# Optimization experiments

Hardware: AMD Instinct MI355X
Metric: run time of the kernel (lower is better)

## Reference

```python
import jax, jax.numpy as jnp
import numpy as np

B, T_HIST, T_OUT, T_FC = 4096, 168, 48, 49
N_LABELS, F_CTL, F_FC, HID = 64, 16, 8, 32
EPS = 1e-7


def setup_inputs() -> dict:
    key = jax.random.key(0)
    ks = jax.random.split(key, 18)
    rn = lambda k, s, sc=1.0: jax.random.normal(k, s, jnp.float32) * sc
    return {
        "history": rn(ks[0], (B, T_HIST, N_LABELS)),
        "control": rn(ks[1], (B, T_OUT, F_CTL)),
        "forecasts": rn(ks[2], (B, T_FC, F_FC)),
        "h_mean": rn(ks[3], (N_LABELS,), 0.1),
        "h_var": jax.random.uniform(ks[4], (N_LABELS,), jnp.float32, 0.5, 1.5),
        "c_mean": rn(ks[5], (F_CTL,), 0.1),
        "c_var": jax.random.uniform(ks[6], (F_CTL,), jnp.float32, 0.5, 1.5),
        "f_mean": rn(ks[7], (), 0.1),
        "f_var": jax.random.uniform(ks[8], (), jnp.float32, 0.5, 1.5),
        "conv_w": rn(ks[9], (2, F_FC, 4), 0.2),   # kernel_size=2, Conv1D(4)
        "conv_b": rn(ks[10], (4,), 0.01),
        "lstm_k": rn(ks[11], (N_LABELS, 4 * HID), 0.1),
        "lstm_rk": rn(ks[12], (HID, 4 * HID), 0.1),
        "lstm_b": rn(ks[13], (4 * HID,), 0.01),
        "w1": rn(ks[14], (HID + F_CTL + 4, 64), 0.1),
        "b1": rn(ks[15], (64,), 0.01),
        "w2": rn(ks[16], (64, N_LABELS), 0.05),
        "b2": rn(ks[17], (N_LABELS,), 0.01),
    }


def _norm(x, m, v):
    # keras Normalization: (x - mean) / max(sqrt(var), eps)
    return (x - m) / jnp.maximum(jnp.sqrt(v), EPS)


def _lstm(x, h, c, k, rk, b):
    z = x @ k + h @ rk + b                      # [B, 4*HID], gate order i,f,g,o
    i, f, g, o = jnp.split(z, 4, axis=-1)
    c2 = jax.nn.sigmoid(f) * c + jax.nn.sigmoid(i) * jnp.tanh(g)
    h2 = jax.nn.sigmoid(o) * jnp.tanh(c2)
    return h2, c2


def _mlp(x1, x2, x3, w1, b1, w2, b2):
    x = jnp.concatenate([x1, x2, x3], axis=-1)  # [B, 52]
    return jax.nn.relu(x @ w1 + b1) @ w2 + b2


def reference(history, control, forecasts, h_mean, h_var, c_mean, c_var,
              f_mean, f_var, conv_w, conv_b, lstm_k, lstm_rk, lstm_b,
              w1, b1, w2, b2):
    latest = history[:, -1, :]                               # [B, N_LABELS]
    cn = _norm(control, c_mean, c_var)                       # [B, T_OUT, F_CTL]
    fn = _norm(forecasts, f_mean, f_var)                     # scalar norm
    # Conv1D(filters=4, kernel_size=2), valid padding -> [B, T_FC-1, 4]
    fc = fn[:, :-1] @ conv_w[0] + fn[:, 1:] @ conv_w[1] + conv_b

    # encoder LSTM over normalized history
    hn = _norm(history, h_mean, h_var)
    bsz = history.shape[0]
    init = (jnp.zeros((bsz, HID), hn.dtype), jnp.zeros((bsz, HID), hn.dtype))

    def enc_step(carry, x):
        h, c = carry
        return _lstm(x, h, c, lstm_k, lstm_rk, lstm_b), None

    (h, c), _ = jax.lax.scan(enc_step, init, jnp.swapaxes(hn, 0, 1))

    # pre-loop step (its prediction write is overwritten by loop i=0, but it
    # updates `latest` which feeds the loop)
    latest = latest + _mlp(h, cn[:, 0], fc[:, 0], w1, b1, w2, b2)

    t_out = control.shape[1]

    def dec_step(carry, inp):
        latest, h, c = carry
        ctl, fci = inp
        xn = _norm(latest, h_mean, h_var)
        h2, c2 = _lstm(xn, h, c, lstm_k, lstm_rk, lstm_b)
        latest2 = latest + _mlp(h2, ctl, fci, w1, b1, w2, b2)
        return (latest2, h2, c2), latest2

    xs = (jnp.swapaxes(cn, 0, 1), jnp.swapaxes(fc[:, :t_out], 0, 1))
    _, preds = jax.lax.scan(dec_step, (latest, h, c), xs)   # [T_OUT, B, N]
    return jnp.swapaxes(preds, 0, 1)                        # [B, T_OUT, N]
```

## Files before the change

kernel.cpp:

```cpp
#include <hip/hip_runtime.h>

#define EPSV 1e-7f

typedef __bf16 bf16x8 __attribute__((ext_vector_type(8)));
typedef float  f32x4  __attribute__((ext_vector_type(4)));
typedef unsigned int   u32x4 __attribute__((ext_vector_type(4)));
typedef unsigned short u16x8 __attribute__((ext_vector_type(8)));
typedef unsigned short u16x4 __attribute__((ext_vector_type(4)));

__device__ __forceinline__ unsigned short f2bf(float f) {
    unsigned int u = __float_as_uint(f);
    return (unsigned short)((u + 0x7FFFu + ((u >> 16) & 1u)) >> 16);
}
__device__ __forceinline__ float bf2f(unsigned short u) {
    return __uint_as_float(((unsigned int)u) << 16);
}
__device__ __forceinline__ void split2(float f, unsigned short& hi, unsigned short& lo) {
    hi = f2bf(f);
    lo = f2bf(f - bf2f(hi));
}
__device__ __forceinline__ void splitT(float f, unsigned short& hi, unsigned short& lo) {
    unsigned int u  = __float_as_uint(f);
    unsigned int hb = u & 0xFFFF0000u;
    float l = f - __uint_as_float(hb);
    hi = (unsigned short)(u >> 16);
    lo = (unsigned short)(__float_as_uint(l) >> 16);
}
__device__ __forceinline__ float sigf(float x) {
    return __builtin_amdgcn_rcpf(1.0f + __expf(-x));
}
__device__ __forceinline__ float tanhfast(float x) {
    float cx = fminf(fmaxf(x, -15.0f), 15.0f);
    float e = __expf(2.0f * cx);
    return (e - 1.0f) * __builtin_amdgcn_rcpf(e + 1.0f);
}
__device__ __forceinline__ float xor8(float v) {
    return __builtin_bit_cast(float, __builtin_amdgcn_update_dpp(
        0, __builtin_bit_cast(int, v), 0x128, 0xF, 0xF, true));
}

#define MFMA16(A, B, C) __builtin_amdgcn_mfma_f32_16x16x32_bf16(A, B, C, 0, 0, 0)
#define BC8(x) __builtin_bit_cast(bf16x8, x)

#define BARRIER() do {                                        \
    asm volatile("s_waitcnt lgkmcnt(0)" ::: "memory");        \
    __builtin_amdgcn_s_barrier();                             \
    __builtin_amdgcn_sched_barrier(0);                        \
} while (0)

#define HS2 72
#define MS  136
#define XS2 136
#define ZS3 20

__global__ __launch_bounds__(512, 1) void tutina_kernel(
    const float* __restrict__ history, const float* __restrict__ control,
    const float* __restrict__ forecasts,
    const float* __restrict__ h_mean, const float* __restrict__ h_var,
    const float* __restrict__ c_mean, const float* __restrict__ c_var,
    const float* __restrict__ f_mean, const float* __restrict__ f_var,
    const float* __restrict__ conv_w, const float* __restrict__ conv_b,
    const float* __restrict__ lstm_k, const float* __restrict__ lstm_rk,
    const float* __restrict__ lstm_b,
    const float* __restrict__ w1, const float* __restrict__ b1,
    const float* __restrict__ w2, const float* __restrict__ b2,
    float* __restrict__ out)
{
    __shared__ unsigned short hbuf[2][16 * HS2];
    __shared__ float zxb[2][4][2][16 * ZS3];
    __shared__ unsigned short xbuf[16 * XS2];
    __shared__ unsigned short mlps[16 * MS];
    __shared__ unsigned short hids[16 * MS];
    __shared__ unsigned int   fcs[48 * 64];

    const int tid  = threadIdx.x;
    const int lane = tid & 63;
    const int wid  = tid >> 6;
    const int wa   = wid & 3;
    const bool gA  = (wid < 4);
    const int lt   = tid & 255;
    const int l15  = lane & 15;
    const int l4   = lane >> 4;
    const int b0   = blockIdx.x * 16;

    for (int i = tid; i < 16 * HS2; i += 512) hbuf[0][i] = 0;
    for (int i = tid; i < 16 * MS;  i += 512) mlps[i] = 0;

    const int  uu     = l15 & 7;
    const bool lohalf = (l15 < 8);
    const int  u      = wa * 8 + uu;
    const int  jz0    = lohalf ? u      : 32 + u;
    const int  jz1    = lohalf ? 64 + u : 96 + u;
    const int  j1     = wa * 16 + l15;

    auto bfragK = [&](int kbase, int j, float& dacc, bf16x8& H, bf16x8& L) {
        u16x8 h, l;
#pragma unroll
        for (int i = 0; i < 8; i++) {
            int k = kbase + l4 * 8 + i;
            float sv = 1.0f / fmaxf(sqrtf(h_var[k]), EPSV);
            float w  = lstm_k[k * 128 + j] * sv;
            dacc += h_mean[k] * w;
            unsigned short hh, ll; split2(w, hh, ll);
            h[i] = hh; l[i] = ll;
        }
        H = BC8(h); L = BC8(l);
    };
    auto bfragP = [&](const float* W, int ldw, int kbase, int j, bf16x8& H, bf16x8& L) {
        u16x8 h, l;
#pragma unroll
        for (int i = 0; i < 8; i++) {
            int k = kbase + l4 * 8 + i;
            float w = W[k * ldw + j];
            unsigned short hh, ll; split2(w, hh, ll);
            h[i] = hh; l[i] = ll;
        }
        H = BC8(h); L = BC8(l);
    };
    auto bfragW11 = [&](int j, float& dacc, bf16x8& H, bf16x8& L) {
        u16x8 h, l;
#pragma unroll
        for (int i = 0; i < 8; i++) {
            int k = 32 + l4 * 8 + i;
            float w = 0.0f;
            if (k < 52) {
                w = w1[k * 64 + j];
                if (k < 48) {
                    float sv = 1.0f / fmaxf(sqrtf(c_var[k - 32]), EPSV);
                    w *= sv;
                    dacc += c_mean[k - 32] * w;
                }
            }
            unsigned short hh, ll; split2(w, hh, ll);
            h[i] = hh; l[i] = ll;
        }
        H = BC8(h); L = BC8(l);
    };

    bf16x8 fA0h, fA0l, fA1h, fA1l, fB0h, fB0l, fB1h, fB1l;
    float dz0 = 0.f, dz1 = 0.f;
    bfragK(0,  jz0, dz0, fA0h, fA0l);
    bfragK(32, jz0, dz0, fA1h, fA1l);
    bfragK(0,  jz1, dz1, fB0h, fB0l);
    bfragK(32, jz1, dz1, fB1h, fB1l);

    bf16x8 fA2h, fA2l, fB2h, fB2l;
    float bi_ = 0.f, bf_ = 0.f, bg_ = 0.f, bo_ = 0.f;
    if (gA) {
        bfragP(lstm_rk, 128, 0, jz0, fA2h, fA2l);
        bfragP(lstm_rk, 128, 0, jz1, fB2h, fB2l);
        float z0s = dz0, z1s = dz1;
        z0s += __shfl_xor(z0s, 16, 64); z0s += __shfl_xor(z0s, 32, 64);
        z1s += __shfl_xor(z1s, 16, 64); z1s += __shfl_xor(z1s, 32, 64);
        float pd0 = xor8(z0s), pd1 = xor8(z1s);
        bi_ = lstm_b[u]      - (lohalf ? z0s : pd0);
        bf_ = lstm_b[32 + u] - (lohalf ? pd0 : z0s);
        bg_ = lstm_b[64 + u] - (lohalf ? z1s : pd1);
        bo_ = lstm_b[96 + u] - (lohalf ? pd1 : z1s);
    }

    bf16x8 fW10h, fW10l, fW11h, fW11l, fW20h, fW20l, fW21h, fW21l;
    float b1j = 0.f, b2j = 0.f;
    float lat0 = 0.f, lat1 = 0.f, lat2 = 0.f, lat3 = 0.f;
    f32x4 creg = {0.f, 0.f, 0.f, 0.f};
    const int rc = lt >> 2, cc = (lt & 3) * 4;
    if (!gA) {
        bfragP(w1, 64, 0, j1, fW10h, fW10l);
        float d1 = 0.f;
        bfragW11(j1, d1, fW11h, fW11l);
        bfragP(w2, 64, 0,  j1, fW20h, fW20l);
        bfragP(w2, 64, 32, j1, fW21h, fW21l);
        d1 += __shfl_xor(d1, 16, 64); d1 += __shfl_xor(d1, 32, 64);
        b1j = b1[j1] - d1;
        b2j = b2[j1];
        lat0 = history[((size_t)(b0 + l4 * 4 + 0) * 168 + 167) * 64 + j1];
        lat1 = history[((size_t)(b0 + l4 * 4 + 1) * 168 + 167) * 64 + j1];
        lat2 = history[((size_t)(b0 + l4 * 4 + 2) * 168 + 167) * 64 + j1];
        lat3 = history[((size_t)(b0 + l4 * 4 + 3) * 168 + 167) * 64 + j1];
        if (lt < 64)
            creg = *(const f32x4*)(control + ((size_t)(b0 + rc) * 48 + 0) * 16 + cc);
        float fm  = f_mean[0];
        float fsc = 1.0f / fmaxf(sqrtf(f_var[0]), EPSV);
        for (int cell = lt; cell < 48 * 64; cell += 256) {
            int t  = cell >> 6;
            int b  = (cell >> 2) & 15;
            int uc = cell & 3;
            const float* fp = forecasts + ((size_t)(b0 + b) * 49 + t) * 8;
            float acc = conv_b[uc];
#pragma unroll
            for (int k = 0; k < 8; k++) {
                acc += (fp[k]     - fm) * fsc * conv_w[k * 4 + uc];
                acc += (fp[8 + k] - fm) * fsc * conv_w[32 + k * 4 + uc];
            }
            unsigned short hh, ll; split2(acc, hh, ll);
            fcs[cell] = ((unsigned int)hh << 16) | ll;
        }
    }

    const int r0 = l4 * 4 + (lohalf ? 0 : 2);
    const int r1 = r0 + 1;
    float c0 = 0.0f, c1 = 0.0f;

    auto lstm_gates = [&](const f32x4& a, const f32x4& b,
                          unsigned short* hw, bool write_mlp) {
        float sa0 = lohalf ? a[2] : a[0];
        float sa1 = lohalf ? a[3] : a[1];
        float sb0 = lohalf ? b[2] : b[0];
        float sb1 = lohalf ? b[3] : b[1];
        float ra0 = xor8(sa0);
        float ra1 = xor8(sa1);
        float rb0 = xor8(sb0);
        float rb1 = xor8(sb1);
        float zi0 = (lohalf ? a[0] : ra0) + bi_;
        float zi1 = (lohalf ? a[1] : ra1) + bi_;
        float zf0 = (lohalf ? ra0 : a[2]) + bf_;
        float zf1 = (lohalf ? ra1 : a[3]) + bf_;
        float zg0 = (lohalf ? b[0] : rb0) + bg_;
        float zg1 = (lohalf ? b[1] : rb1) + bg_;
        float zo0 = (lohalf ? rb0 : b[2]) + bo_;
        float zo1 = (lohalf ? rb1 : b[3]) + bo_;
        c0 = sigf(zf0) * c0 + sigf(zi0) * tanhfast(zg0);
        c1 = sigf(zf1) * c1 + sigf(zi1) * tanhfast(zg1);
        float h20 = sigf(zo0) * tanhfast(c0);
        float h21 = sigf(zo1) * tanhfast(c1);
        unsigned short bh, bl;
        splitT(h20, bh, bl);
        hw[r0 * HS2 + u]      = bh;
        hw[r0 * HS2 + 32 + u] = bl;
        if (write_mlp) { mlps[r0 * MS + u] = bh; mlps[r0 * MS + 64 + u] = bl; }
        splitT(h21, bh, bl);
        hw[r1 * HS2 + u]      = bh;
        hw[r1 * HS2 + 32 + u] = bl;
        if (write_mlp) { mlps[r1 * MS + u] = bh; mlps[r1 * MS + 64 + u] = bl; }
    };

    auto mk_frags = [&](const f32x4& p0, const f32x4& p1, const f32x4& p2,
                        const f32x4& p3, bf16x8& A0h, bf16x8& A0l,
                        bf16x8& A1h, bf16x8& A1l) {
        u16x8 xh_, xl_;
        unsigned short hh, ll;
#pragma unroll
        for (int i = 0; i < 4; i++) { splitT(p0[i], hh, ll); xh_[i] = hh; xl_[i] = ll; }
#pragma unroll
        for (int i = 0; i < 4; i++) { splitT(p1[i], hh, ll); xh_[4+i] = hh; xl_[4+i] = ll; }
        A0h = BC8(xh_); A0l = BC8(xl_);
#pragma unroll
        for (int i = 0; i < 4; i++) { splitT(p2[i], hh, ll); xh_[i] = hh; xl_[i] = ll; }
#pragma unroll
        for (int i = 0; i < 4; i++) { splitT(p3[i], hh, ll); xh_[4+i] = hh; xl_[4+i] = ll; }
        A1h = BC8(xh_); A1l = BC8(xl_);
    };
    auto zx12 = [&](bf16x8 A0h, bf16x8 A0l, bf16x8 A1h, bf16x8 A1l,
                    f32x4& zn0, f32x4& zn1) {
        f32x4 s0 = {0.f,0.f,0.f,0.f}, s1 = {0.f,0.f,0.f,0.f};
        s0 = MFMA16(A0h, fA0h, s0);  s1 = MFMA16(A0h, fB0h, s1);
        s0 = MFMA16(A1h, fA1h, s0);  s1 = MFMA16(A1h, fB1h, s1);
        s0 = MFMA16(A0l, fA0h, s0);  s1 = MFMA16(A0l, fB0h, s1);
        s0 = MFMA16(A1l, fA1h, s0);  s1 = MFMA16(A1l, fB1h, s1);
        s0 = MFMA16(A0h, fA0l, s0);  s1 = MFMA16(A0h, fB0l, s1);
        s0 = MFMA16(A1h, fA1l, s0);  s1 = MFMA16(A1h, fB1l, s1);
        zn0 = s0; zn1 = s1;
    };

    const float* hp = history + (size_t)(b0 + l15) * (168 * 64);
    const int o1 = l4 * 8, o2 = 32 + l4 * 8;
    const int zoff = l15 * ZS3 + l4 * 4;
    f32x4 vb0, vb1, vb2, vb3;
    if (!gA) {
        f32x4 p0 = *(const f32x4*)(hp + o1), p1 = *(const f32x4*)(hp + o1 + 4);
        f32x4 p2 = *(const f32x4*)(hp + o2), p3 = *(const f32x4*)(hp + o2 + 4);
        bf16x8 A0h, A0l, A1h, A1l;
        mk_frags(p0, p1, p2, p3, A0h, A0l, A1h, A1l);
        f32x4 zn0, zn1;
        zx12(A0h, A0l, A1h, A1l, zn0, zn1);
        *(f32x4*)&zxb[0][wa][0][zoff] = zn0;
        *(f32x4*)&zxb[0][wa][1][zoff] = zn1;
        vb0 = *(const f32x4*)(hp + 64 + o1); vb1 = *(const f32x4*)(hp + 64 + o1 + 4);
        vb2 = *(const f32x4*)(hp + 64 + o2); vb3 = *(const f32x4*)(hp + 64 + o2 + 4);
    }
    if (gA) __builtin_amdgcn_s_setprio(1);
    BARRIER();

    for (int t = 0; t < 168; ++t) {
        const int p = t & 1;
        if (gA) {
            const unsigned short* hr = hbuf[p];
            bf16x8 a2h = BC8(*(const u32x4*)&hr[l15 * HS2 + l4 * 8]);
            bf16x8 a2l = BC8(*(const u32x4*)&hr[l15 * HS2 + 32 + l4 * 8]);
            f32x4 z0 = *(const f32x4*)&zxb[p][wa][0][zoff];
            f32x4 z1 = *(const f32x4*)&zxb[p][wa][1][zoff];
            z0 = MFMA16(a2h, fA2h, z0);  z1 = MFMA16(a2h, fB2h, z1);
            z0 = MFMA16(a2l, fA2h, z0);  z1 = MFMA16(a2l, fB2h, z1);
            z0 = MFMA16(a2h, fA2l, z0);  z1 = MFMA16(a2h, fB2l, z1);
            lstm_gates(z0, z1, hbuf[p ^ 1], t == 167);
        } else {
            bf16x8 A0h, A0l, A1h, A1l;
            mk_frags(vb0, vb1, vb2, vb3, A0h, A0l, A1h, A1l);
            const float* np = hp + (size_t)((t < 166) ? t + 2 : 167) * 64;
            vb0 = *(const f32x4*)(np + o1); vb1 = *(const f32x4*)(np + o1 + 4);
            vb2 = *(const f32x4*)(np + o2); vb3 = *(const f32x4*)(np + o2 + 4);
            f32x4 zn0, zn1;
            zx12(A0h, A0l, A1h, A1l, zn0, zn1);
            *(f32x4*)&zxb[p ^ 1][wa][0][zoff] = zn0;
            *(f32x4*)&zxb[p ^ 1][wa][1][zoff] = zn1;
        }
        BARRIER();
    }

    auto stage_cn = [&](const f32x4& v) {
        if (lt < 64) {
            u16x4 oh, ol;
#pragma unroll
            for (int q = 0; q < 4; q++) {
                unsigned short hh, ll;
                splitT(v[q], hh, ll);
                oh[q] = hh; ol[q] = ll;
            }
            *(u16x4*)&mlps[rc * MS + 32 + cc]      = oh;
            *(u16x4*)&mlps[rc * MS + 64 + 32 + cc] = ol;
        }
    };
    auto stage_fc = [&](int t) {
        if (lt >= 64 && lt < 128) {
            int q = lt - 64;
            unsigned int v = fcs[t * 64 + q];
            mlps[(q >> 2) * MS + 48 + (q & 3)]      = (unsigned short)(v >> 16);
            mlps[(q >> 2) * MS + 64 + 48 + (q & 3)] = (unsigned short)(v & 0xFFFFu);
        }
    };
    auto mlp1 = [&]() {
        const int mbase = l15 * MS + l4 * 8;
        bf16x8 m0  = BC8(*(const u32x4*)&mlps[mbase]);
        bf16x8 m1  = BC8(*(const u32x4*)&mlps[mbase + 32]);
        bf16x8 m0l = BC8(*(const u32x4*)&mlps[mbase + 64]);
        bf16x8 m1l = BC8(*(const u32x4*)&mlps[mbase + 96]);
        f32x4 ha = {0.f,0.f,0.f,0.f}, hb = {0.f,0.f,0.f,0.f};
        ha = MFMA16(m0,  fW10h, ha);   hb = MFMA16(m1,  fW11h, hb);
        ha = MFMA16(m0l, fW10h, ha);   hb = MFMA16(m1l, fW11h, hb);
        ha = MFMA16(m0,  fW10l, ha);   hb = MFMA16(m1,  fW11l, hb);
        f32x4 hacc = ha + hb;
#pragma unroll
        for (int q = 0; q < 4; q++) {
            float hv = fmaxf(hacc[q] + b1j, 0.0f);
            unsigned short hh, ll;
            splitT(hv, hh, ll);
            hids[(l4 * 4 + q) * MS + j1]      = hh;
            hids[(l4 * 4 + q) * MS + 64 + j1] = ll;
        }
    };
    auto mlp2 = [&]() {
        const int mbase = l15 * MS + l4 * 8;
        bf16x8 h0  = BC8(*(const u32x4*)&hids[mbase]);
        bf16x8 h1  = BC8(*(const u32x4*)&hids[mbase + 32]);
        bf16x8 h0l = BC8(*(const u32x4*)&hids[mbase + 64]);
        bf16x8 h1l = BC8(*(const u32x4*)&hids[mbase + 96]);
        f32x4 oa = {0.f,0.f,0.f,0.f}, ob = {0.f,0.f,0.f,0.f};
        oa = MFMA16(h0,  fW20h, oa);   ob = MFMA16(h1,  fW21h, ob);
        oa = MFMA16(h0l, fW20h, oa);   ob = MFMA16(h1l, fW21h, ob);
        oa = MFMA16(h0,  fW20l, oa);   ob = MFMA16(h1,  fW21l, ob);
        f32x4 oacc = oa + ob;
        lat0 += oacc[0] + b2j;
        lat1 += oacc[1] + b2j;
        lat2 += oacc[2] + b2j;
        lat3 += oacc[3] + b2j;
    };

    if (!gA) { stage_cn(creg); stage_fc(0); }
    BARRIER();
    if (!gA) mlp1();
    BARRIER();
    if (!gA) mlp2();

    for (int t = 0; t < 48; ++t) {
        const int p = t & 1;
        if (!gA) {
            unsigned short bh, bl;
            splitT(lat0, bh, bl);
            xbuf[(l4 * 4 + 0) * XS2 + j1] = bh; xbuf[(l4 * 4 + 0) * XS2 + 64 + j1] = bl;
            splitT(lat1, bh, bl);
            xbuf[(l4 * 4 + 1) * XS2 + j1] = bh; xbuf[(l4 * 4 + 1) * XS2 + 64 + j1] = bl;
            splitT(lat2, bh, bl);
            xbuf[(l4 * 4 + 2) * XS2 + j1] = bh; xbuf[(l4 * 4 + 2) * XS2 + 64 + j1] = bl;
            splitT(lat3, bh, bl);
            xbuf[(l4 * 4 + 3) * XS2 + j1] = bh; xbuf[(l4 * 4 + 3) * XS2 + 64 + j1] = bl;
            stage_cn(creg);
            stage_fc(t);
            int tn = (t < 47) ? t + 1 : 47;
            if (lt < 64)
                creg = *(const f32x4*)(control + ((size_t)(b0 + rc) * 48 + tn) * 16 + cc);
        }
        BARRIER();

        if (gA) {
            const unsigned short* hr = hbuf[p];
            const int xb = l15 * XS2 + l4 * 8;
            bf16x8 a0h = BC8(*(const u32x4*)&xbuf[xb]);
            bf16x8 a1h = BC8(*(const u32x4*)&xbuf[xb + 32]);
            bf16x8 a0l = BC8(*(const u32x4*)&xbuf[xb + 64]);
            bf16x8 a1l = BC8(*(const u32x4*)&xbuf[xb + 96]);
            bf16x8 a2h = BC8(*(const u32x4*)&hr[l15 * HS2 + l4 * 8]);
            bf16x8 a2l = BC8(*(const u32x4*)&hr[l15 * HS2 + 32 + l4 * 8]);
            f32x4 z0a = {0.f,0.f,0.f,0.f}, z0b = {0.f,0.f,0.f,0.f};
            f32x4 z1a = {0.f,0.f,0.f,0.f}, z1b = {0.f,0.f,0.f,0.f};
            z0a = MFMA16(a0h, fA0h, z0a);  z1a = MFMA16(a0h, fB0h, z1a);
            z0b = MFMA16(a1h, fA1h, z0b);  z1b = MFMA16(a1h, fB1h, z1b);
            z0a = MFMA16(a2h, fA2h, z0a);  z1a = MFMA16(a2h, fB2h, z1a);
            z0b = MFMA16(a0l, fA0h, z0b);  z1b = MFMA16(a0l, fB0h, z1b);
            z0a = MFMA16(a1l, fA1h, z0a);  z1a = MFMA16(a1l, fB1h, z1a);
            z0b = MFMA16(a2l, fA2h, z0b);  z1b = MFMA16(a2l, fB2h, z1b);
            z0a = MFMA16(a0h, fA0l, z0a);  z1a = MFMA16(a0h, fB0l, z1a);
            z0b = MFMA16(a1h, fA1l, z0b);  z1b = MFMA16(a1h, fB1l, z1b);
            z0a = MFMA16(a2h, fA2l, z0a);  z1a = MFMA16(a2h, fB2l, z1a);
            f32x4 z0 = z0a + z0b, z1 = z1a + z1b;
            lstm_gates(z0, z1, hbuf[p ^ 1], true);
        }
        BARRIER();

        if (!gA) mlp1();
        BARRIER();

        if (!gA) {
            mlp2();
            out[((size_t)(b0 + l4 * 4 + 0) * 48 + t) * 64 + j1] = lat0;
            out[((size_t)(b0 + l4 * 4 + 1) * 48 + t) * 64 + j1] = lat1;
            out[((size_t)(b0 + l4 * 4 + 2) * 48 + t) * 64 + j1] = lat2;
            out[((size_t)(b0 + l4 * 4 + 3) * 48 + t) * 64 + j1] = lat3;
        }
    }
}

extern "C" void kernel_launch(void* const* d_in, const int* in_sizes, int n_in,
                              void* d_out, int out_size, void* d_ws, size_t ws_size,
                              hipStream_t stream) {
    tutina_kernel<<<dim3(256), dim3(512), 0, stream>>>(
        (const float*)d_in[0],  (const float*)d_in[1],  (const float*)d_in[2],
        (const float*)d_in[3],  (const float*)d_in[4],  (const float*)d_in[5],
        (const float*)d_in[6],  (const float*)d_in[7],  (const float*)d_in[8],
        (const float*)d_in[9],  (const float*)d_in[10], (const float*)d_in[11],
        (const float*)d_in[12], (const float*)d_in[13], (const float*)d_in[14],
        (const float*)d_in[15], (const float*)d_in[16], (const float*)d_in[17],
        (float*)d_out);
}
```

Baseline: 170.0 us.

## Move decoder MLP2 to LSTM warps, drop one per-step barrier, trim encoder h-lo MFMAs

Moves the second MLP layer and the running 'latest' state from the MLP warp group into the LSTM warps, with each LSTM warp holding w2 fragments for all 64 outputs. The x-staging now happens inside the LSTM phase behind a local LDS wait, which removes one block barrier per decoder step. The encoder recurrence drops the low-half bf16 correction term of h (fewer MFMAs and LDS writes), which lowers precision. The launch-bounds occupancy hint is raised to 2 blocks, which changes register-allocation pressure. The LSTM warps now repeat the MLP2 work redundantly, which adds register use.

```diff
diff --git a/kernel.cpp b/kernel.cpp
--- a/kernel.cpp
+++ b/kernel.cpp
@@ -47,13 +47,17 @@
     __builtin_amdgcn_s_barrier();                             \
     __builtin_amdgcn_sched_barrier(0);                        \
 } while (0)
+#define LGKM0() do {                                          \
+    asm volatile("s_waitcnt lgkmcnt(0)" ::: "memory");        \
+    __builtin_amdgcn_sched_barrier(0);                        \
+} while (0)
 
 #define HS2 72
 #define MS  136
 #define XS2 136
 #define ZS3 20
 
-__global__ __launch_bounds__(512, 1) void tutina_kernel(
+__global__ __launch_bounds__(512, 2) void tutina_kernel(
     const float* __restrict__ history, const float* __restrict__ control,
     const float* __restrict__ forecasts,
     const float* __restrict__ h_mean, const float* __restrict__ h_var,
@@ -145,6 +149,9 @@
     bfragK(32, jz1, dz1, fB1h, fB1l);
 
     bf16x8 fA2h, fA2l, fB2h, fB2l;
+    bf16x8 w2h0[4], w2l0[4], w2h1[4], w2l1[4];
+    float b2jm[4];
+    float lat[4][4];
     float bi_ = 0.f, bf_ = 0.f, bg_ = 0.f, bo_ = 0.f;
     if (gA) {
         bfragP(lstm_rk, 128, 0, jz0, fA2h, fA2l);
@@ -157,26 +164,24 @@
         bf_ = lstm_b[32 + u] - (lohalf ? pd0 : z0s);
         bg_ = lstm_b[64 + u] - (lohalf ? z1s : pd1);
         bo_ = lstm_b[96 + u] - (lohalf ? pd1 : z1s);
-    }
-
-    bf16x8 fW10h, fW10l, fW11h, fW11l, fW20h, fW20l, fW21h, fW21l;
-    float b1j = 0.f, b2j = 0.f;
-    float lat0 = 0.f, lat1 = 0.f, lat2 = 0.f, lat3 = 0.f;
+#pragma unroll
+        for (int m = 0; m < 4; ++m) {
+            bfragP(w2, 64, 0,  m * 16 + l15, w2h0[m], w2l0[m]);
+            bfragP(w2, 64, 32, m * 16 + l15, w2h1[m], w2l1[m]);
+            b2jm[m] = b2[m * 16 + l15];
+        }
+    }
+
+    bf16x8 fW10h, fW10l, fW11h, fW11l;
+    float b1j = 0.f;
     f32x4 creg = {0.f, 0.f, 0.f, 0.f};
     const int rc = lt >> 2, cc = (lt & 3) * 4;
     if (!gA) {
         bfragP(w1, 64, 0, j1, fW10h, fW10l);
         float d1 = 0.f;
         bfragW11(j1, d1, fW11h, fW11l);
-        bfragP(w2, 64, 0,  j1, fW20h, fW20l);
-        bfragP(w2, 64, 32, j1, fW21h, fW21l);
         d1 += __shfl_xor(d1, 16, 64); d1 += __shfl_xor(d1, 32, 64);
         b1j = b1[j1] - d1;
-        b2j = b2[j1];
-        lat0 = history[((size_t)(b0 + l4 * 4 + 0) * 168 + 167) * 64 + j1];
-        lat1 = history[((size_t)(b0 + l4 * 4 + 1) * 168 + 167) * 64 + j1];
-        lat2 = history[((size_t)(b0 + l4 * 4 + 2) * 168 + 167) * 64 + j1];
-        lat3 = history[((size_t)(b0 + l4 * 4 + 3) * 168 + 167) * 64 + j1];
         if (lt < 64)
             creg = *(const f32x4*)(control + ((size_t)(b0 + rc) * 48 + 0) * 16 + cc);
         float fm  = f_mean[0];
@@ -201,8 +206,8 @@
     const int r1 = r0 + 1;
     float c0 = 0.0f, c1 = 0.0f;
 
-    auto lstm_gates = [&](const f32x4& a, const f32x4& b,
-                          unsigned short* hw, bool write_mlp) {
+    auto lstm_gates = [&](const f32x4& a, const f32x4& b, unsigned short* hw,
+                          bool write_lo, bool write_mlp) {
         float sa0 = lohalf ? a[2] : a[0];
         float sa1 = lohalf ? a[3] : a[1];
         float sb0 = lohalf ? b[2] : b[0];
@@ -225,12 +230,12 @@
         float h21 = sigf(zo1) * tanhfast(c1);
         unsigned short bh, bl;
         splitT(h20, bh, bl);
-        hw[r0 * HS2 + u]      = bh;
-        hw[r0 * HS2 + 32 + u] = bl;
+        hw[r0 * HS2 + u] = bh;
+        if (write_lo)  hw[r0 * HS2 + 32 + u] = bl;
         if (write_mlp) { mlps[r0 * MS + u] = bh; mlps[r0 * MS + 64 + u] = bl; }
         splitT(h21, bh, bl);
-        hw[r1 * HS2 + u]      = bh;
-        hw[r1 * HS2 + 32 + u] = bl;
+        hw[r1 * HS2 + u] = bh;
+        if (write_lo)  hw[r1 * HS2 + 32 + u] = bl;
         if (write_mlp) { mlps[r1 * MS + u] = bh; mlps[r1 * MS + 64 + u] = bl; }
     };
 
@@ -286,13 +291,11 @@
         if (gA) {
             const unsigned short* hr = hbuf[p];
             bf16x8 a2h = BC8(*(const u32x4*)&hr[l15 * HS2 + l4 * 8]);
-            bf16x8 a2l = BC8(*(const u32x4*)&hr[l15 * HS2 + 32 + l4 * 8]);
             f32x4 z0 = *(const f32x4*)&zxb[p][wa][0][zoff];
             f32x4 z1 = *(const f32x4*)&zxb[p][wa][1][zoff];
             z0 = MFMA16(a2h, fA2h, z0);  z1 = MFMA16(a2h, fB2h, z1);
-            z0 = MFMA16(a2l, fA2h, z0);  z1 = MFMA16(a2l, fB2h, z1);
             z0 = MFMA16(a2h, fA2l, z0);  z1 = MFMA16(a2h, fB2l, z1);
-            lstm_gates(z0, z1, hbuf[p ^ 1], t == 167);
+            lstm_gates(z0, z1, hbuf[p ^ 1], t == 167, t == 167);
         } else {
             bf16x8 A0h, A0l, A1h, A1l;
             mk_frags(vb0, vb1, vb2, vb3, A0h, A0l, A1h, A1l);
@@ -305,6 +308,15 @@
             *(f32x4*)&zxb[p ^ 1][wa][1][zoff] = zn1;
         }
         BARRIER();
+    }
+
+    if (gA) {
+#pragma unroll
+        for (int m = 0; m < 4; ++m)
+#pragma unroll
+            for (int q = 0; q < 4; ++q)
+                lat[m][q] = history[((size_t)(b0 + l4 * 4 + q) * 168 + 167) * 64
+                                    + m * 16 + l15];
     }
 
     auto stage_cn = [&](const f32x4& v) {
@@ -348,50 +360,44 @@
             hids[(l4 * 4 + q) * MS + 64 + j1] = ll;
         }
     };
-    auto mlp2 = [&]() {
+    auto mlp2A = [&]() {
         const int mbase = l15 * MS + l4 * 8;
         bf16x8 h0  = BC8(*(const u32x4*)&hids[mbase]);
         bf16x8 h1  = BC8(*(const u32x4*)&hids[mbase + 32]);
         bf16x8 h0l = BC8(*(const u32x4*)&hids[mbase + 64]);
         bf16x8 h1l = BC8(*(const u32x4*)&hids[mbase + 96]);
-        f32x4 oa = {0.f,0.f,0.f,0.f}, ob = {0.f,0.f,0.f,0.f};
-        oa = MFMA16(h0,  fW20h, oa);   ob = MFMA16(h1,  fW21h, ob);
-        oa = MFMA16(h0l, fW20h, oa);   ob = MFMA16(h1l, fW21h, ob);
-        oa = MFMA16(h0,  fW20l, oa);   ob = MFMA16(h1,  fW21l, ob);
-        f32x4 oacc = oa + ob;
-        lat0 += oacc[0] + b2j;
-        lat1 += oacc[1] + b2j;
-        lat2 += oacc[2] + b2j;
-        lat3 += oacc[3] + b2j;
+#pragma unroll
+        for (int m = 0; m < 4; ++m) {
+            f32x4 oa = {0.f,0.f,0.f,0.f}, ob = {0.f,0.f,0.f,0.f};
+            oa = MFMA16(h0,  w2h0[m], oa);   ob = MFMA16(h1,  w2h1[m], ob);
+            oa = MFMA16(h0l, w2h0[m], oa);   ob = MFMA16(h1l, w2h1[m], ob);
+            oa = MFMA16(h0,  w2l0[m], oa);   ob = MFMA16(h1,  w2l1[m], ob);
+            f32x4 o = oa + ob;
+#pragma unroll
+            for (int q = 0; q < 4; ++q)
+                lat[m][q] += o[q] + b2jm[m];
+        }
     };
 
     if (!gA) { stage_cn(creg); stage_fc(0); }
     BARRIER();
     if (!gA) mlp1();
     BARRIER();
-    if (!gA) mlp2();
+    if (gA) mlp2A();
 
     for (int t = 0; t < 48; ++t) {
         const int p = t & 1;
-        if (!gA) {
-            unsigned short bh, bl;
-            splitT(lat0, bh, bl);
-            xbuf[(l4 * 4 + 0) * XS2 + j1] = bh; xbuf[(l4 * 4 + 0) * XS2 + 64 + j1] = bl;
-            splitT(lat1, bh, bl);
-            xbuf[(l4 * 4 + 1) * XS2 + j1] = bh; xbuf[(l4 * 4 + 1) * XS2 + 64 + j1] = bl;
-            splitT(lat2, bh, bl);
-            xbuf[(l4 * 4 + 2) * XS2 + j1] = bh; xbuf[(l4 * 4 + 2) * XS2 + 64 + j1] = bl;
-            splitT(lat3, bh, bl);
-            xbuf[(l4 * 4 + 3) * XS2 + j1] = bh; xbuf[(l4 * 4 + 3) * XS2 + 64 + j1] = bl;
-            stage_cn(creg);
-            stage_fc(t);
-            int tn = (t < 47) ? t + 1 : 47;
-            if (lt < 64)
-                creg = *(const f32x4*)(control + ((size_t)(b0 + rc) * 48 + tn) * 16 + cc);
-        }
-        BARRIER();
-
         if (gA) {
+#pragma unroll
+            for (int m = 0; m < 4; ++m)
+#pragma unroll
+                for (int q = 0; q < 4; ++q) {
+                    unsigned short bh, bl;
+                    splitT(lat[m][q], bh, bl);
+                    xbuf[(l4 * 4 + q) * XS2 + m * 16 + l15]      = bh;
+                    xbuf[(l4 * 4 + q) * XS2 + 64 + m * 16 + l15] = bl;
+                }
+            LGKM0();
             const unsigned short* hr = hbuf[p];
             const int xb = l15 * XS2 + l4 * 8;
             bf16x8 a0h = BC8(*(const u32x4*)&xbuf[xb]);
@@ -412,19 +418,25 @@
             z0b = MFMA16(a1h, fA1l, z0b);  z1b = MFMA16(a1h, fB1l, z1b);
             z0a = MFMA16(a2h, fA2l, z0a);  z1a = MFMA16(a2h, fB2l, z1a);
             f32x4 z0 = z0a + z0b, z1 = z1a + z1b;
-            lstm_gates(z0, z1, hbuf[p ^ 1], true);
+            lstm_gates(z0, z1, hbuf[p ^ 1], true, true);
+        } else {
+            stage_cn(creg);
+            stage_fc(t);
+            int tn = (t < 47) ? t + 1 : 47;
+            if (lt < 64)
+                creg = *(const f32x4*)(control + ((size_t)(b0 + rc) * 48 + tn) * 16 + cc);
         }
         BARRIER();
 
         if (!gA) mlp1();
         BARRIER();
 
-        if (!gA) {
-            mlp2();
-            out[((size_t)(b0 + l4 * 4 + 0) * 48 + t) * 64 + j1] = lat0;
-            out[((size_t)(b0 + l4 * 4 + 1) * 48 + t) * 64 + j1] = lat1;
-            out[((size_t)(b0 + l4 * 4 + 2) * 48 + t) * 64 + j1] = lat2;
-            out[((size_t)(b0 + l4 * 4 + 3) * 48 + t) * 64 + j1] = lat3;
+        if (gA) {
+            mlp2A();
+#pragma unroll
+            for (int q = 0; q < 4; ++q)
+                out[((size_t)(b0 + l4 * 4 + q) * 48 + t) * 64 + wa * 16 + l15]
+                    = lat[wa][q];
         }
     }
 }
```

New measurement: 197.4 us. 1.16x slower.
